# Performance work log

Measured on AMD Instinct MI355X. Metric: run time of the kernel, lower is better.

## Reference

```python
import jax, jax.numpy as jnp
import numpy as np

B, N, K = 4, 512, 10
PI_SCALE = 0.05  # keeps sum_k pi in (0, 0.5) so the [1e-8, 1] clamp does not saturate at 1
MCMC_KEY = jax.random.key(42)


def setup_inputs() -> dict:
    key = jax.random.key(0)
    k1, k2, k3, k4 = jax.random.split(key, 4)
    mu = jax.random.normal(k1, (B, N, K), dtype=jnp.float32)
    sig = jax.random.uniform(k2, (B, N, K), dtype=jnp.float32)
    pi = jax.random.uniform(k3, (B, N, K), dtype=jnp.float32) * PI_SCALE
    A_0 = jax.random.uniform(k4, (N, N), dtype=jnp.float32)
    return {"mu": mu, "sig": sig, "pi": pi, "A_0": A_0, "num_samples": 100}


def reference(mu, sig, pi, A_0, num_samples):
    b, n, k = mu.shape

    # Mixture-weighted proposal mean/std:  sum_k softmax(pi)_k * {mu,sig}_k
    component_probs = jax.nn.softmax(pi, axis=-1)          # [B,N,K]
    selected_mu = jnp.sum(component_probs * mu, axis=-1)    # [B,N]
    selected_sig = jnp.sum(component_probs * sig, axis=-1)  # [B,N]

    # edge_probs[b,i,j] = clamp(sum_k pi[b,i,k]) -- constant in j; hoisted out of the loop
    # since it depends only on pi (the torch code recomputes it every step).
    edge_probs = jnp.clip(jnp.sum(pi, axis=2), 1e-8, 1.0)[:, :, None]  # [B,N,1]
    log_ep = jnp.log(edge_probs)                                        # [B,N,1]
    log_1mep = jnp.log(1.0 - edge_probs)                                # [B,N,1]

    def log_likelihood(A):  # A: [B,N,N] -> [N]  (sum over dims 0,1 as in torch)
        return jnp.sum(A * log_ep + (1.0 - A) * log_1mep, axis=(0, 1))

    def step(carry, t):
        current_A, acc = carry
        kk = jax.random.fold_in(MCMC_KEY, t)
        k_noise, k_unif = jax.random.split(kk)
        noise = jax.random.normal(k_noise, (b, n), dtype=selected_mu.dtype)
        proposed_mu = selected_mu + noise * selected_sig              # [B,N]
        # sigmoid of rank-1 outer product: einsum('bnc,bmc->bnm') with c==1
        proposed_A = jax.nn.sigmoid(proposed_mu[:, :, None] * proposed_mu[:, None, :])
        ratio = jnp.mean(jnp.clip(jnp.exp(log_likelihood(proposed_A) - log_likelihood(current_A)), 0.0, 1.0))
        accept = jax.random.uniform(k_unif, (b,)) < ratio             # [B] bool
        current_A = jnp.where(accept[:, None, None], proposed_A, current_A)
        return (current_A, acc + current_A), None

    cur0 = jnp.broadcast_to(A_0, (b, n, n)).astype(mu.dtype)
    acc0 = jnp.zeros((b, n, n), dtype=mu.dtype)
    (_, acc), _ = jax.lax.scan(step, (cur0, acc0), jnp.arange(num_samples))
    return acc / num_samples
```

## Files before the change

kernel.cpp:

```cpp
#include <hip/hip_runtime.h>
#include <stdint.h>

#define T_STEPS 100
#define BB 4
#define NN 512
#define KK 10
#define LOG2E 1.4426950408889634

typedef float f4 __attribute__((ext_vector_type(4)));

__device__ __forceinline__ uint32_t rotl32(uint32_t v, int d) {
  return (v << d) | (v >> (32 - d));
}

__device__ __forceinline__ void tf2x32(uint32_t k0, uint32_t k1,
                                       uint32_t& x0, uint32_t& x1) {
  uint32_t k2 = k0 ^ k1 ^ 0x1BD11BDAu;
  x0 += k0; x1 += k1;
#define TFR(r) { x0 += x1; x1 = rotl32(x1, r); x1 ^= x0; }
  TFR(13) TFR(15) TFR(26) TFR(6)   x0 += k1; x1 += k2 + 1u;
  TFR(17) TFR(29) TFR(16) TFR(24)  x0 += k2; x1 += k0 + 2u;
  TFR(13) TFR(15) TFR(26) TFR(6)   x0 += k0; x1 += k1 + 3u;
  TFR(17) TFR(29) TFR(16) TFR(24)  x0 += k1; x1 += k2 + 4u;
  TFR(13) TFR(15) TFR(26) TFR(6)   x0 += k2; x1 += k0 + 5u;
#undef TFR
}

__device__ __forceinline__ float bits_to_u01(uint32_t bits) {
  return __fsub_rn(__uint_as_float((bits >> 9) | 0x3f800000u), 1.0f);
}

__device__ __forceinline__ float erfinv_f32(float x) {
  float w = -logf(__fmul_rn(__fsub_rn(1.0f, x), __fadd_rn(1.0f, x)));
  float p;
  if (w < 5.0f) {
    w = __fsub_rn(w, 2.5f);
    p = 2.81022636e-08f;
    p = __fadd_rn(__fmul_rn(p, w), 3.43273939e-07f);
    p = __fadd_rn(__fmul_rn(p, w), -3.5233877e-06f);
    p = __fadd_rn(__fmul_rn(p, w), -4.39150654e-06f);
    p = __fadd_rn(__fmul_rn(p, w), 0.00021858087f);
    p = __fadd_rn(__fmul_rn(p, w), -0.00125372503f);
    p = __fadd_rn(__fmul_rn(p, w), -0.00417768164f);
    p = __fadd_rn(__fmul_rn(p, w), 0.246640727f);
    p = __fadd_rn(__fmul_rn(p, w), 1.50140941f);
  } else {
    w = __fsub_rn(sqrtf(w), 3.0f);
    p = -0.000200214257f;
    p = __fadd_rn(__fmul_rn(p, w), 0.000100950558f);
    p = __fadd_rn(__fmul_rn(p, w), 0.00134934322f);
    p = __fadd_rn(__fmul_rn(p, w), -0.00367342844f);
    p = __fadd_rn(__fmul_rn(p, w), 0.00573950773f);
    p = __fadd_rn(__fmul_rn(p, w), -0.0076224613f);
    p = __fadd_rn(__fmul_rn(p, w), 0.00943887047f);
    p = __fadd_rn(__fmul_rn(p, w), 1.00167406f);
    p = __fadd_rn(__fmul_rn(p, w), 2.83297682f);
  }
  return __fmul_rn(p, x);
}

__device__ __forceinline__ float fast_sigmoid(float x) {
  float e = __expf(-x);
  return __builtin_amdgcn_rcpf(__fadd_rn(1.0f, e));
}

template <int CTRL>
__device__ __forceinline__ float dpp_add(float x) {
  int v = __builtin_amdgcn_update_dpp(0, __float_as_int(x), CTRL, 0xF, 0xF, true);
  return __fadd_rn(x, __int_as_float(v));
}

__global__ void rng_kernel(const float* __restrict__ mu,
                           const float* __restrict__ sig,
                           const float* __restrict__ pi,
                           float* __restrict__ pm, float* __restrict__ uacc,
                           float* __restrict__ Lf) {
  int id = blockIdx.x * blockDim.x + threadIdx.x;
  if (id >= T_STEPS * BB * NN) return;
  int t = id >> 11;
  int m = id & 2047;

  const float* pp = pi + m * KK;
  float mx = pp[0];
  for (int k = 1; k < KK; k++) mx = fmaxf(mx, pp[k]);
  float e[KK]; float s = 0.0f;
  for (int k = 0; k < KK; k++) { e[k] = expf(__fsub_rn(pp[k], mx)); s = __fadd_rn(s, e[k]); }
  float smv = 0.0f, ssv = 0.0f, eps = 0.0f;
  for (int k = 0; k < KK; k++) {
    float p = e[k] / s;
    smv = __fadd_rn(smv, __fmul_rn(p, mu[m * KK + k]));
    ssv = __fadd_rn(ssv, __fmul_rn(p, sig[m * KK + k]));
    eps = __fadd_rn(eps, pp[k]);
  }
  if (t == 0) {
    float ep = fminf(fmaxf(eps, 1e-8f), 1.0f);
    float lep = logf(ep);
    float l1 = logf(__fsub_rn(1.0f, ep));
    Lf[m] = (float)((double)lep - (double)l1);
  }

  uint32_t kk0 = 0u, kk1 = (uint32_t)t;
  tf2x32(0u, 42u, kk0, kk1);
  uint32_t n0 = 0u, n1 = 0u; tf2x32(kk0, kk1, n0, n1);
  uint32_t y0 = 0u, y1 = (uint32_t)m;
  tf2x32(n0, n1, y0, y1);
  uint32_t bits = y0 ^ y1;

  float u01 = bits_to_u01(bits);
  const float lo = -0.99999994f;
  float u = fmaxf(lo, __fadd_rn(__fmul_rn(u01, 2.0f), lo));
  float z = __fmul_rn(1.41421356237309515f, erfinv_f32(u));
  pm[id] = __fadd_rn(smv, __fmul_rn(z, ssv));

  if (m < 4) {
    uint32_t u0 = 0u, u1 = 1u; tf2x32(kk0, kk1, u0, u1);
    uint32_t c0 = 0u, c1 = (uint32_t)m;
    tf2x32(u0, u1, c0, c1);
    uacc[t * 4 + m] = __fmul_rn(bits_to_u01(c0 ^ c1), 512.0f);
  }
}

__global__ __launch_bounds__(512) void ll_kernel(const float* __restrict__ pm,
                                                 const float* __restrict__ Lf,
                                                 const float* __restrict__ A0,
                                                 float* __restrict__ llt,
                                                 float* __restrict__ ll0) {
  __shared__ float spm[NN];
  __shared__ float sLc[NN];
  __shared__ double pt[4][128];
  int tid = threadIdx.x;
  int q = tid >> 7, jj = tid & 127;
  int bi = blockIdx.x;
  if (bi < 1600) {
    int tb = bi >> 2, jc = bi & 3;
    int b = tb & 3;
    spm[tid] = pm[tb * NN + tid];
    sLc[tid] = Lf[b * NN + tid];
    __syncthreads();
    int j = jc * 128 + jj;
    float pmj = spm[j];
    int i0 = q * 128;
    double acc = 0.0;
    #pragma unroll 8
    for (int i = 0; i < 128; i += 2) {
      float x0 = __fmul_rn(spm[i0 + i], pmj);
      float x1 = __fmul_rn(spm[i0 + i + 1], pmj);
      float t0 = __fmul_rn(fast_sigmoid(x0), sLc[i0 + i]);
      float t1 = __fmul_rn(fast_sigmoid(x1), sLc[i0 + i + 1]);
      acc += (double)__fadd_rn(t0, t1);
    }
    pt[q][jj] = acc;
    __syncthreads();
    if (tid < 128) {
      double a = ((pt[0][jj] + pt[1][jj]) + pt[2][jj]) + pt[3][jj];
      llt[tb * NN + jc * 128 + jj] = (float)(a * LOG2E);
    }
  } else {
    int idx = bi - 1600;
    int b = idx >> 2, jc = idx & 3;
    sLc[tid] = Lf[b * NN + tid];
    __syncthreads();
    int j = jc * 128 + jj;
    int i0 = q * 128;
    double acc = 0.0;
    #pragma unroll 4
    for (int i = 0; i < 128; i++) {
      acc += (double)A0[(size_t)(i0 + i) * NN + j] * (double)sLc[i0 + i];
    }
    pt[q][jj] = acc;
    __syncthreads();
    if (tid < 128) {
      double a = ((pt[0][jj] + pt[1][jj]) + pt[2][jj]) + pt[3][jj];
      ll0[b * NN + jc * 128 + jj] = (float)(a * LOG2E);
    }
  }
}

#define CH_LOAD(P, T)                                                        \
  {                                                                          \
    _Pragma("unroll")                                                        \
    for (int b = 0; b < 4; b++) {                                            \
      _Pragma("unroll")                                                      \
      for (int k = 0; k < 2; k++)                                            \
        P[b * 2 + k] = lltv[((size_t)(T) * 4 + b) * 128 + k * 64 + g];       \
    }                                                                        \
  }

#define CH_STEP(P, T)                                                        \
  {                                                                          \
    float4 ua = uaccv[T];                                                    \
    f4 tp0 = (P[0] + P[2]) + (P[4] + P[6]);                                  \
    f4 tp1 = (P[1] + P[3]) + (P[5] + P[7]);                                  \
    f4 d0 = tp0 - S0;                                                        \
    f4 d1 = tp1 - S1;                                                        \
    f4 E0, E1;                                                               \
    _Pragma("unroll")                                                        \
    for (int c = 0; c < 4; c++) {                                            \
      E0[c] = fminf(exp2f(d0[c]), 1.0f);                                     \
      E1[c] = fminf(exp2f(d1[c]), 1.0f);                                     \
    }                                                                        \
    f4 Es = E0 + E1;                                                         \
    float ps = __fadd_rn(__fadd_rn(Es[0], Es[1]), __fadd_rn(Es[2], Es[3]));  \
    ps = dpp_add<0xB1>(ps);                                        \
    ps = dpp_add<0x4E>(ps);                                        \
    ps = dpp_add<0x141>(ps);                         \
    ps = dpp_add<0x140>(ps);                              \
    ps = __fadd_rn(ps, __int_as_float(__builtin_amdgcn_ds_swizzle(           \
             __float_as_int(ps), 0x401F)));                       \
    ps = __fadd_rn(ps, __int_as_float(__builtin_amdgcn_ds_bpermute(          \
             lx32, __float_as_int(ps))));                         \
    if (ua.x < ps) { st0 = (T); cur[0] = P[0]; cur[1] = P[1]; }              \
    if (ua.y < ps) { st1 = (T); cur[2] = P[2]; cur[3] = P[3]; }              \
    if (ua.z < ps) { st2 = (T); cur[4] = P[4]; cur[5] = P[5]; }              \
    if (ua.w < ps) { st3 = (T); cur[6] = P[6]; cur[7] = P[7]; }              \
    S0 = (cur[0] + cur[2]) + (cur[4] + cur[6]);                              \
    S1 = (cur[1] + cur[3]) + (cur[5] + cur[7]);                              \
    if (g == 0) {                                                            \
      uint32_t pk = (uint32_t)(st0 + 1) | ((uint32_t)(st1 + 1) << 8) |       \
                    ((uint32_t)(st2 + 1) << 16) | ((uint32_t)(st3 + 1) << 24);\
      spk[T] = pk;                                                           \
    }                                                                        \
  }

__global__ __launch_bounds__(64, 1) void chain_kernel(const float* __restrict__ llt,
                                                      const float* __restrict__ ll0,
                                                      const float* __restrict__ uacc,
                                                      int* __restrict__ slist,
                                                      float* __restrict__ wlist,
                                                      int* __restrict__ Mv) {
  __shared__ uint32_t spk[T_STEPS];
  __shared__ int scnt[BB][101];
  int g = threadIdx.x;
  int lx32 = (g ^ 32) << 2;

  const f4* lltv = (const f4*)llt;
  const f4* ll0v = (const f4*)ll0;
  const float4* uaccv = (const float4*)uacc;

  f4 cur[8];
  #pragma unroll
  for (int b = 0; b < 4; b++)
    #pragma unroll
    for (int k = 0; k < 2; k++) cur[b * 2 + k] = ll0v[b * 128 + k * 64 + g];
  f4 S0 = (cur[0] + cur[2]) + (cur[4] + cur[6]);
  f4 S1 = (cur[1] + cur[3]) + (cur[5] + cur[7]);
  int st0 = -1, st1 = -1, st2 = -1, st3 = -1;

  f4 Pa[8], Pb[8], Pc[8];
  CH_LOAD(Pa, 0)
  CH_LOAD(Pb, 1)
  CH_LOAD(Pc, 2)

  for (int t = 0; t < 99; t += 3) {
    CH_STEP(Pa, t)
    if (t + 3 < T_STEPS) CH_LOAD(Pa, t + 3)
    CH_STEP(Pb, t + 1)
    if (t + 4 < T_STEPS) CH_LOAD(Pb, t + 4)
    CH_STEP(Pc, t + 2)
    if (t + 5 < T_STEPS) CH_LOAD(Pc, t + 5)
  }
  CH_STEP(Pa, 99)

  __syncthreads();
  for (int s = g; s < BB * 101; s += 64) (&scnt[0][0])[s] = 0;
  __syncthreads();
  {
    uint32_t p0 = spk[g];
    atomicAdd(&scnt[0][p0 & 255], 1);
    atomicAdd(&scnt[1][(p0 >> 8) & 255], 1);
    atomicAdd(&scnt[2][(p0 >> 16) & 255], 1);
    atomicAdd(&scnt[3][p0 >> 24], 1);
    if (g < T_STEPS - 64) {
      uint32_t p1 = spk[64 + g];
      atomicAdd(&scnt[0][p1 & 255], 1);
      atomicAdd(&scnt[1][(p1 >> 8) & 255], 1);
      atomicAdd(&scnt[2][(p1 >> 16) & 255], 1);
      atomicAdd(&scnt[3][p1 >> 24], 1);
    }
  }
  __syncthreads();
  if (g < 4) {
    int m = 0;
    for (int s = 0; s <= 100; s++) {
      int c = scnt[g][s];
      if (c) { slist[g * 104 + m] = s; wlist[g * 104 + m] = (float)c; m++; }
    }
    Mv[g] = m;
  }
}

__global__ __launch_bounds__(512) void out_kernel(const float* __restrict__ pm,
                                                  const float* __restrict__ A0,
                                                  const int* __restrict__ slist,
                                                  const float* __restrict__ wlist,
                                                  const int* __restrict__ Mv,
                                                  float* __restrict__ out) {
  int b = blockIdx.x >> 9;
  int i = blockIdx.x & 511;
  int j = threadIdx.x;
  int M = Mv[b];
  float r = 0.0f;
  for (int e = 0; e < M; e++) {
    int s = slist[b * 104 + e];
    float w = wlist[b * 104 + e];
    if (s == 0) {
      r += w * A0[(size_t)i * NN + j];
    } else {
      int t = s - 1;
      float pmi = pm[(size_t)(t * BB + b) * NN + i];
      float pmj = pm[(size_t)(t * BB + b) * NN + j];
      r += w * fast_sigmoid(__fmul_rn(pmi, pmj));
    }
  }
  out[((size_t)b * NN + i) * NN + j] = r * 0.01f;
}

extern "C" void kernel_launch(void* const* d_in, const int* in_sizes, int n_in,
                              void* d_out, int out_size, void* d_ws, size_t ws_size,
                              hipStream_t stream) {
  const float* mu  = (const float*)d_in[0];
  const float* sig = (const float*)d_in[1];
  const float* pi  = (const float*)d_in[2];
  const float* A0  = (const float*)d_in[3];

  char* ws = (char*)d_ws;
  size_t off = 0;
  auto alloc = [&](size_t bytes) -> char* {
    char* p = ws + off;
    off += (bytes + 255) & ~(size_t)255;
    return p;
  };
  float* llt   = (float*)alloc((size_t)T_STEPS * BB * NN * 4);
  float* ll0   = (float*)alloc(BB * NN * 4);
  float* pm    = (float*)alloc((size_t)T_STEPS * BB * NN * 4);
  float* Lf    = (float*)alloc(BB * NN * 4);
  float* uacc  = (float*)alloc(T_STEPS * 4 * 4);
  int*   slist = (int*)alloc(BB * 104 * 4);
  float* wlist = (float*)alloc(BB * 104 * 4);
  int*   Mv    = (int*)alloc(4 * 4);
  float* outp  = (float*)d_out;

  rng_kernel<<<(T_STEPS * BB * NN + 255) / 256, 256, 0, stream>>>(mu, sig, pi,
                                                                  pm, uacc, Lf);
  ll_kernel<<<1616, 512, 0, stream>>>(pm, Lf, A0, llt, ll0);
  chain_kernel<<<1, 64, 0, stream>>>(llt, ll0, uacc, slist, wlist, Mv);
  out_kernel<<<BB * NN, 512, 0, stream>>>(pm, A0, slist, wlist, Mv, outp);
}
```

Measured before the change: 145.9 us.

## Precompute per-step batch-summed log-likelihoods and shorten serial chain step

The ll_kernel now processes all four batches of a timestep in one block and also writes the batch-summed proposed log-likelihood per column (tsum), so the serial chain kernel no longer sums four proposals each step. The chain step replaces the swizzle/bpermute cross-half reduction with four readlane calls, makes the accept mask wave-uniform, and only recomputes the current sum when something is accepted. Uniforms are staged in LDS and the prefetch depth drops from three buffers to two. This shortens the single-wave critical path but cuts ll_kernel's grid from 1616 to 416 blocks, leaving each block four serialized batch passes with extra barriers and less parallelism.

```diff
diff --git a/kernel.cpp b/kernel.cpp
--- a/kernel.cpp
+++ b/kernel.cpp
@@ -69,6 +69,9 @@
   int v = __builtin_amdgcn_update_dpp(0, __float_as_int(x), CTRL, 0xF, 0xF, true);
   return __fadd_rn(x, __int_as_float(v));
 }
+__device__ __forceinline__ float readlane_f(float x, int lane) {
+  return __int_as_float(__builtin_amdgcn_readlane(__float_as_int(x), lane));
+}
 
 __global__ void rng_kernel(const float* __restrict__ mu,
                            const float* __restrict__ sig,
@@ -124,48 +127,56 @@
                                                  const float* __restrict__ Lf,
                                                  const float* __restrict__ A0,
                                                  float* __restrict__ llt,
-                                                 float* __restrict__ ll0) {
-  __shared__ float spm[NN];
-  __shared__ float sLc[NN];
+                                                 float* __restrict__ ll0,
+                                                 float* __restrict__ tsum) {
+  __shared__ float spm[BB][NN];
+  __shared__ float sL[BB][NN];
   __shared__ double pt[4][128];
   int tid = threadIdx.x;
   int q = tid >> 7, jj = tid & 127;
   int bi = blockIdx.x;
-  if (bi < 1600) {
-    int tb = bi >> 2, jc = bi & 3;
-    int b = tb & 3;
-    spm[tid] = pm[tb * NN + tid];
-    sLc[tid] = Lf[b * NN + tid];
+  if (bi < 400) {
+    int t = bi >> 2, jc = bi & 3;
+    #pragma unroll
+    for (int b = 0; b < BB; b++) {
+      spm[b][tid] = pm[(t * 4 + b) * NN + tid];
+      sL[b][tid] = Lf[b * NN + tid];
+    }
     __syncthreads();
-    int j = jc * 128 + jj;
-    float pmj = spm[j];
     int i0 = q * 128;
-    double acc = 0.0;
-    #pragma unroll 8
-    for (int i = 0; i < 128; i += 2) {
-      float x0 = __fmul_rn(spm[i0 + i], pmj);
-      float x1 = __fmul_rn(spm[i0 + i + 1], pmj);
-      float t0 = __fmul_rn(fast_sigmoid(x0), sLc[i0 + i]);
-      float t1 = __fmul_rn(fast_sigmoid(x1), sLc[i0 + i + 1]);
-      acc += (double)__fadd_rn(t0, t1);
-    }
-    pt[q][jj] = acc;
-    __syncthreads();
-    if (tid < 128) {
-      double a = ((pt[0][jj] + pt[1][jj]) + pt[2][jj]) + pt[3][jj];
-      llt[tb * NN + jc * 128 + jj] = (float)(a * LOG2E);
-    }
+    double tsd = 0.0;
+    for (int b = 0; b < BB; b++) {
+      float pmj = spm[b][jc * 128 + jj];
+      double acc = 0.0;
+      #pragma unroll 8
+      for (int i = 0; i < 128; i += 2) {
+        float x0 = __fmul_rn(spm[b][i0 + i], pmj);
+        float x1 = __fmul_rn(spm[b][i0 + i + 1], pmj);
+        float t0 = __fmul_rn(fast_sigmoid(x0), sL[b][i0 + i]);
+        float t1 = __fmul_rn(fast_sigmoid(x1), sL[b][i0 + i + 1]);
+        acc += (double)__fadd_rn(t0, t1);
+      }
+      pt[q][jj] = acc;
+      __syncthreads();
+      if (tid < 128) {
+        double a = ((pt[0][jj] + pt[1][jj]) + pt[2][jj]) + pt[3][jj];
+        llt[(t * 4 + b) * NN + jc * 128 + jj] = (float)(a * LOG2E);
+        tsd += a;
+      }
+      __syncthreads();
+    }
+    if (tid < 128) tsum[t * NN + jc * 128 + jj] = (float)(tsd * LOG2E);
   } else {
-    int idx = bi - 1600;
+    int idx = bi - 400;
     int b = idx >> 2, jc = idx & 3;
-    sLc[tid] = Lf[b * NN + tid];
+    sL[0][tid] = Lf[b * NN + tid];
     __syncthreads();
     int j = jc * 128 + jj;
     int i0 = q * 128;
     double acc = 0.0;
     #pragma unroll 4
     for (int i = 0; i < 128; i++) {
-      acc += (double)A0[(size_t)(i0 + i) * NN + j] * (double)sLc[i0 + i];
+      acc += (double)A0[(size_t)(i0 + i) * NN + j] * (double)sL[0][i0 + i];
     }
     pt[q][jj] = acc;
     __syncthreads();
@@ -176,23 +187,23 @@
   }
 }
 
-#define CH_LOAD(P, T)                                                        \
+#define CH_LOAD(BUF, T)                                                      \
   {                                                                          \
+    BUF##Ts0 = tsv[(size_t)(T) * 128 + g];                                   \
+    BUF##Ts1 = tsv[(size_t)(T) * 128 + 64 + g];                              \
     _Pragma("unroll")                                                        \
     for (int b = 0; b < 4; b++) {                                            \
       _Pragma("unroll")                                                      \
       for (int k = 0; k < 2; k++)                                            \
-        P[b * 2 + k] = lltv[((size_t)(T) * 4 + b) * 128 + k * 64 + g];       \
+        BUF##R[b * 2 + k] = lltv[((size_t)(T) * 4 + b) * 128 + k * 64 + g];  \
     }                                                                        \
   }
 
-#define CH_STEP(P, T)                                                        \
+#define CH_STEP(BUF, T)                                                      \
   {                                                                          \
-    float4 ua = uaccv[T];                                                    \
-    f4 tp0 = (P[0] + P[2]) + (P[4] + P[6]);                                  \
-    f4 tp1 = (P[1] + P[3]) + (P[5] + P[7]);                                  \
-    f4 d0 = tp0 - S0;                                                        \
-    f4 d1 = tp1 - S1;                                                        \
+    float4 ua = sua[T];                                                      \
+    f4 d0 = BUF##Ts0 - C0;                                                   \
+    f4 d1 = BUF##Ts1 - C1;                                                   \
     f4 E0, E1;                                                               \
     _Pragma("unroll")                                                        \
     for (int c = 0; c < 4; c++) {                                            \
@@ -205,16 +216,20 @@
     ps = dpp_add<0x4E>(ps);                                        \
     ps = dpp_add<0x141>(ps);                         \
     ps = dpp_add<0x140>(ps);                              \
-    ps = __fadd_rn(ps, __int_as_float(__builtin_amdgcn_ds_swizzle(           \
-             __float_as_int(ps), 0x401F)));                       \
-    ps = __fadd_rn(ps, __int_as_float(__builtin_amdgcn_ds_bpermute(          \
-             lx32, __float_as_int(ps))));                         \
-    if (ua.x < ps) { st0 = (T); cur[0] = P[0]; cur[1] = P[1]; }              \
-    if (ua.y < ps) { st1 = (T); cur[2] = P[2]; cur[3] = P[3]; }              \
-    if (ua.z < ps) { st2 = (T); cur[4] = P[4]; cur[5] = P[5]; }              \
-    if (ua.w < ps) { st3 = (T); cur[6] = P[6]; cur[7] = P[7]; }              \
-    S0 = (cur[0] + cur[2]) + (cur[4] + cur[6]);                              \
-    S1 = (cur[1] + cur[3]) + (cur[5] + cur[7]);                              \
+    float s0 = readlane_f(ps, 0), s1 = readlane_f(ps, 16);                   \
+    float s2 = readlane_f(ps, 32), s3 = readlane_f(ps, 48);                  \
+    float tot = __fadd_rn(__fadd_rn(s0, s1), __fadd_rn(s2, s3));             \
+    int am = (ua.x < tot ? 1 : 0) | (ua.y < tot ? 2 : 0) |                   \
+             (ua.z < tot ? 4 : 0) | (ua.w < tot ? 8 : 0);                    \
+    am = __builtin_amdgcn_readfirstlane(am);                                 \
+    if (am) {                                                                \
+      if (am & 1) { st0 = (T); cur[0] = BUF##R[0]; cur[1] = BUF##R[1]; }     \
+      if (am & 2) { st1 = (T); cur[2] = BUF##R[2]; cur[3] = BUF##R[3]; }     \
+      if (am & 4) { st2 = (T); cur[4] = BUF##R[4]; cur[5] = BUF##R[5]; }     \
+      if (am & 8) { st3 = (T); cur[6] = BUF##R[6]; cur[7] = BUF##R[7]; }     \
+      C0 = (cur[0] + cur[2]) + (cur[4] + cur[6]);                            \
+      C1 = (cur[1] + cur[3]) + (cur[5] + cur[7]);                            \
+    }                                                                        \
     if (g == 0) {                                                            \
       uint32_t pk = (uint32_t)(st0 + 1) | ((uint32_t)(st1 + 1) << 8) |       \
                     ((uint32_t)(st2 + 1) << 16) | ((uint32_t)(st3 + 1) << 24);\
@@ -223,43 +238,45 @@
   }
 
 __global__ __launch_bounds__(64, 1) void chain_kernel(const float* __restrict__ llt,
+                                                      const float* __restrict__ tsum,
                                                       const float* __restrict__ ll0,
                                                       const float* __restrict__ uacc,
                                                       int* __restrict__ slist,
                                                       float* __restrict__ wlist,
                                                       int* __restrict__ Mv) {
+  __shared__ float4 sua[T_STEPS];
   __shared__ uint32_t spk[T_STEPS];
   __shared__ int scnt[BB][101];
   int g = threadIdx.x;
-  int lx32 = (g ^ 32) << 2;
+
+  const float4* uacc4 = (const float4*)uacc;
+  for (int t = g; t < T_STEPS; t += 64) sua[t] = uacc4[t];
 
   const f4* lltv = (const f4*)llt;
+  const f4* tsv  = (const f4*)tsum;
   const f4* ll0v = (const f4*)ll0;
-  const float4* uaccv = (const float4*)uacc;
 
   f4 cur[8];
   #pragma unroll
   for (int b = 0; b < 4; b++)
     #pragma unroll
     for (int k = 0; k < 2; k++) cur[b * 2 + k] = ll0v[b * 128 + k * 64 + g];
-  f4 S0 = (cur[0] + cur[2]) + (cur[4] + cur[6]);
-  f4 S1 = (cur[1] + cur[3]) + (cur[5] + cur[7]);
+  f4 C0 = (cur[0] + cur[2]) + (cur[4] + cur[6]);
+  f4 C1 = (cur[1] + cur[3]) + (cur[5] + cur[7]);
   int st0 = -1, st1 = -1, st2 = -1, st3 = -1;
 
-  f4 Pa[8], Pb[8], Pc[8];
-  CH_LOAD(Pa, 0)
-  CH_LOAD(Pb, 1)
-  CH_LOAD(Pc, 2)
-
-  for (int t = 0; t < 99; t += 3) {
-    CH_STEP(Pa, t)
-    if (t + 3 < T_STEPS) CH_LOAD(Pa, t + 3)
-    CH_STEP(Pb, t + 1)
-    if (t + 4 < T_STEPS) CH_LOAD(Pb, t + 4)
-    CH_STEP(Pc, t + 2)
-    if (t + 5 < T_STEPS) CH_LOAD(Pc, t + 5)
-  }
-  CH_STEP(Pa, 99)
+  f4 ATs0, ATs1, AR[8];
+  f4 BTs0, BTs1, BR[8];
+  CH_LOAD(A, 0)
+  CH_LOAD(B, 1)
+  __syncthreads();
+
+  for (int t = 0; t < T_STEPS; t += 2) {
+    CH_STEP(A, t)
+    if (t + 2 < T_STEPS) CH_LOAD(A, t + 2)
+    CH_STEP(B, t + 1)
+    if (t + 3 < T_STEPS) CH_LOAD(B, t + 3)
+  }
 
   __syncthreads();
   for (int s = g; s < BB * 101; s += 64) (&scnt[0][0])[s] = 0;
@@ -331,6 +348,7 @@
     return p;
   };
   float* llt   = (float*)alloc((size_t)T_STEPS * BB * NN * 4);
+  float* tsum  = (float*)alloc((size_t)T_STEPS * NN * 4);
   float* ll0   = (float*)alloc(BB * NN * 4);
   float* pm    = (float*)alloc((size_t)T_STEPS * BB * NN * 4);
   float* Lf    = (float*)alloc(BB * NN * 4);
@@ -342,7 +360,7 @@
 
   rng_kernel<<<(T_STEPS * BB * NN + 255) / 256, 256, 0, stream>>>(mu, sig, pi,
                                                                   pm, uacc, Lf);
-  ll_kernel<<<1616, 512, 0, stream>>>(pm, Lf, A0, llt, ll0);
-  chain_kernel<<<1, 64, 0, stream>>>(llt, ll0, uacc, slist, wlist, Mv);
+  ll_kernel<<<416, 512, 0, stream>>>(pm, Lf, A0, llt, ll0, tsum);
+  chain_kernel<<<1, 64, 0, stream>>>(llt, tsum, ll0, uacc, slist, wlist, Mv);
   out_kernel<<<BB * NN, 512, 0, stream>>>(pm, A0, slist, wlist, Mv, outp);
 }
```

Measured after the change: 155.4 us. +6.5%, slower.
